# Kernel optimization log

Measured on AMD Instinct MI355X. Metric: run time of the kernel, lower is better.

## Reference

```python
import jax, jax.numpy as jnp
import numpy as np

B, S, Hd = 2, 2048, 2048
NH, DH = 16, 128
FF = 4 * Hd
EPS = 1e-5


def layer_norm(x, g, b):
    mu = jnp.mean(x, axis=-1, keepdims=True)
    var = jnp.mean(jnp.square(x - mu), axis=-1, keepdims=True)
    return (x - mu) * jax.lax.rsqrt(var + EPS) * g + b


def setup_inputs() -> dict:
    key = jax.random.key(0)
    ks = jax.random.split(key, 10)
    s = lambda n: 1.0 / np.sqrt(n)
    return {
        "hidden_states": jax.random.normal(ks[0], (B, S, Hd), jnp.float32),
        "attention_mask": jnp.zeros((B, S), jnp.float32),
        "ln1_g": jnp.ones((Hd,), jnp.float32),
        "ln1_b": jnp.zeros((Hd,), jnp.float32),
        "ln2_g": jnp.ones((Hd,), jnp.float32),
        "ln2_b": jnp.zeros((Hd,), jnp.float32),
        "Wq": jax.random.normal(ks[1], (Hd, NH * DH), jnp.float32) * s(Hd),
        "Wk": jax.random.normal(ks[2], (Hd, NH * DH), jnp.float32) * s(Hd),
        "Wv": jax.random.normal(ks[3], (Hd, NH * DH), jnp.float32) * s(Hd),
        "Wo": jax.random.normal(ks[4], (NH * DH, Hd), jnp.float32) * s(NH * DH),
        "W1": jax.random.normal(ks[5], (Hd, FF), jnp.float32) * s(Hd),
        "b1": jnp.zeros((FF,), jnp.float32),
        "W2": jax.random.normal(ks[6], (FF, Hd), jnp.float32) * s(FF),
        "b2": jnp.zeros((Hd,), jnp.float32),
    }


def reference(hidden_states, attention_mask, ln1_g, ln1_b, ln2_g, ln2_b,
              Wq, Wk, Wv, Wo, W1, b1, W2, b2):
    x = hidden_states
    # --- attention sub-block ---
    h = layer_norm(x, ln1_g, ln1_b)
    q = (h @ Wq).reshape(B, S, NH, DH)
    k = (h @ Wk).reshape(B, S, NH, DH)
    v = (h @ Wv).reshape(B, S, NH, DH)
    scores = jnp.einsum("bqhd,bkhd->bhqk", q, k) / np.sqrt(DH).astype(np.float32)
    scores = scores + attention_mask[:, None, None, :]  # additive mask
    probs = jax.nn.softmax(scores, axis=-1)
    ctx = jnp.einsum("bhqk,bkhd->bqhd", probs, v).reshape(B, S, NH * DH)
    x = x + ctx @ Wo
    # --- MLP sub-block ---
    h = layer_norm(x, ln2_g, ln2_b)
    h = jax.nn.gelu(h @ W1 + b1, approximate=False)
    x = x + h @ W2 + b2
    return x
```

## Files before the change

kernel.cpp:

```cpp
#include <hip/hip_runtime.h>
#include <math.h>

#define B_ 2
#define S_ 2048
#define HD 2048
#define NH_ 16
#define DH_ 128
#define FF_ 8192
#define MROWS (B_*S_)
#define LDQ 6144

typedef __attribute__((ext_vector_type(8))) short bf16x8;
typedef __attribute__((ext_vector_type(4))) short s16x4;
typedef __attribute__((ext_vector_type(4))) float f32x4;

static __device__ __forceinline__ unsigned short f2bf(float f) {
    unsigned u = __float_as_uint(f);
    u += 0x7fffu + ((u >> 16) & 1u);
    return (unsigned short)(u >> 16);
}

static __device__ __forceinline__ unsigned short f2bf_rna(float f) {
    return (unsigned short)((__float_as_uint(f) + 0x8000u) >> 16);
}

static __device__ __forceinline__ void gload_lds16(const void* g, void* lds) {
    __builtin_amdgcn_global_load_lds((const __attribute__((address_space(1))) void*)g,
                                     (__attribute__((address_space(3))) void*)lds, 16, 0, 0);
}

__global__ __launch_bounds__(256) void trcvt_kernel(const float* __restrict__ W,
        short* __restrict__ Wt, int K, int N) {
    __shared__ float tile[64][65];
    int t = threadIdx.x;
    int tr = t >> 4;
    int tc4 = (t & 15) * 4;
    int r0 = blockIdx.y * 64, c0 = blockIdx.x * 64;
    #pragma unroll
    for (int i = 0; i < 4; i++) {
        float4 v = *(const float4*)(W + (size_t)(r0 + tr + 16*i) * N + c0 + tc4);
        tile[tr + 16*i][tc4 + 0] = v.x;
        tile[tr + 16*i][tc4 + 1] = v.y;
        tile[tr + 16*i][tc4 + 2] = v.z;
        tile[tr + 16*i][tc4 + 3] = v.w;
    }
    __syncthreads();
    #pragma unroll
    for (int i = 0; i < 4; i++) {
        int oc = tr + 16*i;
        s16x4 o;
        o.x = (short)f2bf(tile[tc4 + 0][oc]);
        o.y = (short)f2bf(tile[tc4 + 1][oc]);
        o.z = (short)f2bf(tile[tc4 + 2][oc]);
        o.w = (short)f2bf(tile[tc4 + 3][oc]);
        *(s16x4*)(Wt + (size_t)(c0 + oc) * K + r0 + tc4) = o;
    }
}

__global__ __launch_bounds__(256) void vtrans_kernel(const short* __restrict__ qkv,
        short* __restrict__ vT) {
    __shared__ short tile[32][33];
    int t = threadIdx.x;
    int tx = t & 31, ty = t >> 5;
    int c0 = blockIdx.x * 32;
    int r0 = blockIdx.y * 32;
    int b  = blockIdx.z;
    #pragma unroll
    for (int i = 0; i < 4; i++)
        tile[ty + 8*i][tx] = qkv[(size_t)(b*S_ + r0 + ty + 8*i) * LDQ + 4096 + c0 + tx];
    __syncthreads();
    #pragma unroll
    for (int i = 0; i < 4; i++)
        vT[((size_t)(c0 + ty + 8*i) * 2 + b) * S_ + r0 + tx] = tile[tx][ty + 8*i];
}

__global__ __launch_bounds__(256) void ln_kernel(const float* __restrict__ x,
                const float* __restrict__ g, const float* __restrict__ b,
                short* __restrict__ out) {
    int row = blockIdx.x;
    const float* xr = x + (size_t)row * HD;
    short* orow = out + (size_t)row * HD;
    int t = threadIdx.x;

    float4 v0 = ((const float4*)xr)[t];
    float4 v1 = ((const float4*)xr)[t + 256];
    float s  = v0.x + v0.y + v0.z + v0.w + v1.x + v1.y + v1.z + v1.w;
    float ss = v0.x*v0.x + v0.y*v0.y + v0.z*v0.z + v0.w*v0.w
             + v1.x*v1.x + v1.y*v1.y + v1.z*v1.z + v1.w*v1.w;

    #pragma unroll
    for (int off = 1; off < 64; off <<= 1) {
        s  += __shfl_xor(s,  off, 64);
        ss += __shfl_xor(ss, off, 64);
    }
    __shared__ float ws_s[4], ws_q[4];
    int wid = t >> 6;
    if ((t & 63) == 0) { ws_s[wid] = s; ws_q[wid] = ss; }
    __syncthreads();
    s  = ws_s[0] + ws_s[1] + ws_s[2] + ws_s[3];
    ss = ws_q[0] + ws_q[1] + ws_q[2] + ws_q[3];

    float mu  = s * (1.0f / HD);
    float var = ss * (1.0f / HD) - mu * mu;
    float rs  = rsqrtf(var + 1e-5f);

    float4 g0 = ((const float4*)g)[t];
    float4 g1 = ((const float4*)g)[t + 256];
    float4 b0 = ((const float4*)b)[t];
    float4 b1 = ((const float4*)b)[t + 256];
    s16x4 o0, o1;
    o0.x = (short)f2bf((v0.x - mu) * rs * g0.x + b0.x);
    o0.y = (short)f2bf((v0.y - mu) * rs * g0.y + b0.y);
    o0.z = (short)f2bf((v0.z - mu) * rs * g0.z + b0.z);
    o0.w = (short)f2bf((v0.w - mu) * rs * g0.w + b0.w);
    o1.x = (short)f2bf((v1.x - mu) * rs * g1.x + b1.x);
    o1.y = (short)f2bf((v1.y - mu) * rs * g1.y + b1.y);
    o1.z = (short)f2bf((v1.z - mu) * rs * g1.z + b1.z);
    o1.w = (short)f2bf((v1.w - mu) * rs * g1.w + b1.w);
    ((s16x4*)orow)[t]       = o0;
    ((s16x4*)orow)[t + 256] = o1;
}

template<bool PATCH, bool OUTBF16, bool BIAS, bool RES, bool GELU>
__global__ __launch_bounds__(256, 2) void gemm128(
        const short* __restrict__ A, const short* __restrict__ Bt,
        const float* __restrict__ bias, const float* __restrict__ res,
        void* __restrict__ Cout, int M, int N, int K) {
    __shared__ __align__(16) char ldsA[2][128 * 128];
    __shared__ __align__(16) char ldsB[2][128 * 128];

    int tid = threadIdx.x;
    int wave = tid >> 6, lane = tid & 63;
    int l4 = lane >> 4, lm = lane & 15;
    int wm = wave >> 1, wn = wave & 1;

    int bid = blockIdx.x;
    int m0, n0;
    if constexpr (PATCH) {
        int xcd = bid & 7, local = bid >> 3;
        m0 = ((xcd & 3) * 8 + (local & 7)) << 7;
        n0 = ((xcd >> 2) * 8 + (local >> 3)) << 7;
    } else {
        int nx = N >> 7;
        m0 = (bid / nx) << 7; n0 = (bid % nx) << 7;
    }

    const short* Atile = A + (size_t)m0 * K;
    const short* Btile = Bt + (size_t)n0 * K;
    const int NT = K >> 6;

    auto stage = [&](int t, int buf) {
        int tw = (t >= NT) ? t - NT : t;
        const short* gA = Atile + tw * 64;
        const short* gB = Btile + tw * 64;
        #pragma unroll
        for (int s = 0; s < 4; s++) {
            int n = (wave * 4 + s) * 64 + lane;
            int row = n >> 3, c = n & 7;
            int cs = c ^ (row & 7);
            gload_lds16(gA + (size_t)row * K + cs * 8, ldsA[buf] + n * 16);
            gload_lds16(gB + (size_t)row * K + cs * 8, ldsB[buf] + n * 16);
        }
    };

    int ch0 = (l4) ^ (lm & 7);
    int ch1 = (4 | l4) ^ (lm & 7);
    const char* pA = (const char*)ldsA + (wm * 64 + lm) * 128;
    const char* pB = (const char*)ldsB + (wn * 64 + lm) * 128;

    f32x4 acc[4][4] = {};

    stage(0, 0);
    for (int t = 0; t < NT; t++) {
        int buf = t & 1;
        stage(t + 1, buf ^ 1);
        asm volatile("s_waitcnt vmcnt(8)" ::: "memory");
        __builtin_amdgcn_s_barrier();
        __builtin_amdgcn_sched_barrier(0);
        size_t bo = (size_t)buf * 128 * 128;
        __builtin_amdgcn_s_setprio(1);
        #pragma unroll
        for (int kk = 0; kk < 2; kk++) {
            int ch = kk ? ch1 : ch0;
            bf16x8 av[4], bv[4];
            #pragma unroll
            for (int f = 0; f < 4; f++)
                av[f] = *(const bf16x8*)(pA + bo + f * 2048 + ch * 16);
            #pragma unroll
            for (int nn = 0; nn < 4; nn++)
                bv[nn] = *(const bf16x8*)(pB + bo + nn * 2048 + ch * 16);
            #pragma unroll
            for (int f = 0; f < 4; f++)
                #pragma unroll
                for (int nn = 0; nn < 4; nn++)
                    acc[f][nn] = __builtin_amdgcn_mfma_f32_16x16x32_bf16(
                        av[f], bv[nn], acc[f][nn], 0, 0, 0);
        }
        __builtin_amdgcn_s_setprio(0);
        __builtin_amdgcn_s_barrier();
    }
    asm volatile("s_waitcnt vmcnt(0)" ::: "memory");
    __builtin_amdgcn_s_barrier();

    #pragma unroll
    for (int nn = 0; nn < 4; nn++) {
        int colb = n0 + wn * 64 + nn * 16 + lm;
        float bvs = BIAS ? bias[colb] : 0.f;
        #pragma unroll
        for (int m = 0; m < 4; m++) {
            #pragma unroll
            for (int r = 0; r < 4; r++) {
                int row = m0 + wm * 64 + m * 16 + l4 * 4 + r;
                float v = acc[m][nn][r] + bvs;
                if (GELU) {
                    float y = 1.5957691f * (v + 0.044715f * v * v * v);
                    v = v / (1.0f + __expf(-y));
                }
                size_t off = (size_t)row * N + colb;
                if (RES) v += res[off];
                if (OUTBF16) ((short*)Cout)[off] = (short)f2bf(v);
                else         ((float*)Cout)[off] = v;
            }
        }
    }
}

__global__ __launch_bounds__(256) void attn_kernel(
        const short* __restrict__ qkv, const short* __restrict__ vT,
        const float* __restrict__ mask, short* __restrict__ ctx) {
    __shared__ __align__(16) short Ks[64*128];
    __shared__ __align__(16) short Vt[128*64];
    __shared__ __align__(16) short Ps[4][16*72];
    int t = threadIdx.x;
    int wave = t >> 6, lane = t & 63;
    int l4 = lane >> 4, lm = lane & 15;
    int q0 = blockIdx.x * 64, h = blockIdx.y, zb = blockIdx.z;
    const float scale = 0.08838834764831845f;

    bf16x8 aq[4];
    {
        const short* qrow = qkv + (size_t)(zb*S_ + q0 + wave*16 + lm) * LDQ + h*DH_;
        #pragma unroll
        for (int ks = 0; ks < 4; ks++)
            aq[ks] = *(const bf16x8*)(qrow + ks*32 + l4*8);
    }

    float m_r[4], l_r[4];
    #pragma unroll
    for (int r = 0; r < 4; r++) { m_r[r] = -INFINITY; l_r[r] = 0.f; }
    f32x4 o[8];
    #pragma unroll
    for (int i = 0; i < 8; i++) o[i] = (f32x4){0.f, 0.f, 0.f, 0.f};

    for (int kv0 = 0; kv0 < S_; kv0 += 64) {
        __syncthreads();
        #pragma unroll
        for (int L = 0; L < 4; L++) {
            int c = (wave*4 + L)*64 + lane;
            int krow = c >> 4, kc = c & 15;
            int ksrc = (kc & 8) | ((kc ^ (krow & 7)) & 7);
            gload_lds16(qkv + (size_t)(zb*S_ + kv0 + krow)*LDQ + 2048 + h*DH_ + ksrc*8,
                        (char*)Ks + c*16);
            int drow = c >> 3, dc = c & 7;
            int dsrc = dc ^ (drow & 7);
            gload_lds16(vT + ((size_t)(h*DH_ + drow)*2 + zb)*S_ + kv0 + dsrc*8,
                        (char*)Vt + c*16);
        }
        __syncthreads();

        f32x4 s[4];
        #pragma unroll
        for (int nb = 0; nb < 4; nb++) s[nb] = (f32x4){0.f, 0.f, 0.f, 0.f};
        __builtin_amdgcn_s_setprio(1);
        #pragma unroll
        for (int nb = 0; nb < 4; nb++) {
            int row = nb*16 + lm;
            #pragma unroll
            for (int ks = 0; ks < 4; ks++) {
                bf16x8 bk = *(const bf16x8*)((const char*)Ks +
                              ((row*256 + ks*64 + l4*16) ^ ((row & 7) << 4)));
                s[nb] = __builtin_amdgcn_mfma_f32_16x16x32_bf16(aq[ks], bk, s[nb], 0, 0, 0);
            }
        }
        __builtin_amdgcn_s_setprio(0);

        float mk[4];
        #pragma unroll
        for (int nb = 0; nb < 4; nb++) mk[nb] = mask[(size_t)zb*S_ + kv0 + nb*16 + lm];

        float pv_[4][4], pm[4];
        float need = -1e30f;
        #pragma unroll
        for (int r = 0; r < 4; r++) {
            float vmax = -INFINITY;
            #pragma unroll
            for (int nb = 0; nb < 4; nb++) {
                float v = fmaf(s[nb][r], scale, mk[nb]);
                pv_[r][nb] = v;
                vmax = fmaxf(vmax, v);
            }
            vmax = fmaxf(vmax, __shfl_xor(vmax, 1, 64));
            vmax = fmaxf(vmax, __shfl_xor(vmax, 2, 64));
            vmax = fmaxf(vmax, __shfl_xor(vmax, 4, 64));
            vmax = fmaxf(vmax, __shfl_xor(vmax, 8, 64));
            pm[r] = vmax;
            need = fmaxf(need, vmax - m_r[r]);
        }
        if (!__all(need <= 8.0f)) {
            float fac[4];
            #pragma unroll
            for (int r = 0; r < 4; r++) {
                float nm = fmaxf(m_r[r], pm[r]);
                fac[r] = __expf(m_r[r] - nm);
                l_r[r] *= fac[r];
                m_r[r] = nm;
            }
            #pragma unroll
            for (int i = 0; i < 8; i++)
                #pragma unroll
                for (int r = 0; r < 4; r++) o[i][r] *= fac[r];
        }
        #pragma unroll
        for (int r = 0; r < 4; r++) {
            float ps = 0.f;
            #pragma unroll
            for (int nb = 0; nb < 4; nb++) {
                float e = __expf(pv_[r][nb] - m_r[r]);
                pv_[r][nb] = e;
                ps += e;
            }
            ps += __shfl_xor(ps, 1, 64);
            ps += __shfl_xor(ps, 2, 64);
            ps += __shfl_xor(ps, 4, 64);
            ps += __shfl_xor(ps, 8, 64);
            l_r[r] += ps;
        }

        short* Pw = (short*)Ps[wave];
        #pragma unroll
        for (int r = 0; r < 4; r++)
            #pragma unroll
            for (int nb = 0; nb < 4; nb++)
                Pw[(l4*4 + r)*72 + nb*16 + lm] = (short)f2bf_rna(pv_[r][nb]);

        __builtin_amdgcn_s_setprio(1);
        #pragma unroll
        for (int ks = 0; ks < 2; ks++) {
            bf16x8 ap = *(const bf16x8*)(Pw + lm*72 + ks*32 + l4*8);
            #pragma unroll
            for (int nd = 0; nd < 8; nd++) {
                int d = nd*16 + lm;
                bf16x8 bvv = *(const bf16x8*)((const char*)Vt +
                              (((d*128) + ks*64 + l4*16) ^ ((d & 7) << 4)));
                o[nd] = __builtin_amdgcn_mfma_f32_16x16x32_bf16(ap, bvv, o[nd], 0, 0, 0);
            }
        }
        __builtin_amdgcn_s_setprio(0);
    }

    float inv[4];
    #pragma unroll
    for (int r = 0; r < 4; r++) inv[r] = 1.0f / l_r[r];
    #pragma unroll
    for (int nd = 0; nd < 8; nd++) {
        #pragma unroll
        for (int r = 0; r < 4; r++) {
            size_t row = (size_t)(zb*S_ + q0 + wave*16 + l4*4 + r);
            ctx[row * HD + h*DH_ + nd*16 + lm] = (short)f2bf(o[nd][r] * inv[r]);
        }
    }
}

extern "C" void kernel_launch(void* const* d_in, const int* in_sizes, int n_in,
                              void* d_out, int out_size, void* d_ws, size_t ws_size,
                              hipStream_t stream) {
    const float* x      = (const float*)d_in[0];
    const float* mask   = (const float*)d_in[1];
    const float* ln1_g  = (const float*)d_in[2];
    const float* ln1_b  = (const float*)d_in[3];
    const float* ln2_g  = (const float*)d_in[4];
    const float* ln2_b  = (const float*)d_in[5];
    const float* Wq     = (const float*)d_in[6];
    const float* Wk     = (const float*)d_in[7];
    const float* Wv     = (const float*)d_in[8];
    const float* Wo     = (const float*)d_in[9];
    const float* W1     = (const float*)d_in[10];
    const float* b1     = (const float*)d_in[11];
    const float* W2     = (const float*)d_in[12];
    const float* b2     = (const float*)d_in[13];
    float* out = (float*)d_out;

    char* ws = (char*)d_ws;
    size_t off = 0;
    const size_t WSQ  = (size_t)HD * HD * 2;
    const size_t WFF  = (size_t)HD * FF_ * 2;
    const size_t ACTB = (size_t)MROWS * HD * 2;
    short* WqkvT = (short*)(ws + off); off += 3 * WSQ;
    short* WoT   = (short*)(ws + off); off += WSQ;
    short* W1T   = (short*)(ws + off); off += WFF;
    short* W2T   = (short*)(ws + off); off += WFF;
    short* hb    = (short*)(ws + off); off += ACTB;
    short* qkv   = (short*)(ws + off); off += (size_t)MROWS * LDQ * 2;
    short* vTb   = (short*)(ws + off); off += (size_t)HD * B_ * S_ * 2;
    float* x1    = (float*)(ws + off); off += (size_t)MROWS * HD * 4;
    short* cb    = WqkvT;
    short* act   = qkv;

    dim3 blk(256);

    trcvt_kernel<<<dim3(HD/64,  HD/64),  blk, 0, stream>>>(Wq, WqkvT,                 HD, HD);
    trcvt_kernel<<<dim3(HD/64,  HD/64),  blk, 0, stream>>>(Wk, WqkvT + (size_t)HD*HD, HD, HD);
    trcvt_kernel<<<dim3(HD/64,  HD/64),  blk, 0, stream>>>(Wv, WqkvT + (size_t)2*HD*HD, HD, HD);
    trcvt_kernel<<<dim3(HD/64,  HD/64),  blk, 0, stream>>>(Wo, WoT, HD, HD);
    trcvt_kernel<<<dim3(FF_/64, HD/64),  blk, 0, stream>>>(W1, W1T, HD, FF_);
    trcvt_kernel<<<dim3(HD/64,  FF_/64), blk, 0, stream>>>(W2, W2T, FF_, HD);

    ln_kernel<<<MROWS, blk, 0, stream>>>(x, ln1_g, ln1_b, hb);

    gemm128<false,true,false,false,false><<<dim3((MROWS/128)*(LDQ/128)), 256, 0, stream>>>(
        hb, WqkvT, nullptr, nullptr, qkv, MROWS, LDQ, HD);

    vtrans_kernel<<<dim3(HD/32, S_/32, B_), blk, 0, stream>>>(qkv, vTb);

    attn_kernel<<<dim3(S_/64, NH_, B_), blk, 0, stream>>>(qkv, vTb, mask, cb);

    gemm128<true,false,false,true,false><<<dim3((MROWS/128)*(HD/128)), 256, 0, stream>>>(
        cb, WoT, nullptr, x, x1, MROWS, HD, HD);

    ln_kernel<<<MROWS, blk, 0, stream>>>(x1, ln2_g, ln2_b, hb);

    gemm128<false,true,true,false,true><<<dim3((MROWS/128)*(FF_/128)), 256, 0, stream>>>(
        hb, W1T, b1, nullptr, act, MROWS, FF_, HD);

    gemm128<true,false,true,true,false><<<dim3((MROWS/128)*(HD/128)), 256, 0, stream>>>(
        act, W2T, b2, x1, out, MROWS, HD, FF_);
}
```

Before: 768.2 us.

## Double-buffer K/V tiles in attention to overlap global loads with MFMA

The attention kernel now keeps two LDS buffers for K and V and issues the async global-to-LDS loads for the next tile before computing on the current one. It waits only on the older batch of loads (vmcnt(8)) and uses explicit barriers, so load latency can hide behind the QK and PV MFMAs. The last iteration stages a redundant wrapped-around tile to keep the wait count uniform, which adds one extra tile of traffic. LDS use doubles to about 72KB, which may lower occupancy.

```diff
diff --git a/kernel.cpp b/kernel.cpp
--- a/kernel.cpp
+++ b/kernel.cpp
@@ -228,14 +228,15 @@
 __global__ __launch_bounds__(256) void attn_kernel(
         const short* __restrict__ qkv, const short* __restrict__ vT,
         const float* __restrict__ mask, short* __restrict__ ctx) {
-    __shared__ __align__(16) short Ks[64*128];
-    __shared__ __align__(16) short Vt[128*64];
+    __shared__ __align__(16) short Ks[2][64*128];
+    __shared__ __align__(16) short Vt[2][128*64];
     __shared__ __align__(16) short Ps[4][16*72];
     int t = threadIdx.x;
     int wave = t >> 6, lane = t & 63;
     int l4 = lane >> 4, lm = lane & 15;
     int q0 = blockIdx.x * 64, h = blockIdx.y, zb = blockIdx.z;
     const float scale = 0.08838834764831845f;
+    const int NT = S_ / 64;
 
     bf16x8 aq[4];
     {
@@ -245,28 +246,40 @@
             aq[ks] = *(const bf16x8*)(qrow + ks*32 + l4*8);
     }
 
-    float m_r[4], l_r[4];
-    #pragma unroll
-    for (int r = 0; r < 4; r++) { m_r[r] = -INFINITY; l_r[r] = 0.f; }
-    f32x4 o[8];
-    #pragma unroll
-    for (int i = 0; i < 8; i++) o[i] = (f32x4){0.f, 0.f, 0.f, 0.f};
-
-    for (int kv0 = 0; kv0 < S_; kv0 += 64) {
-        __syncthreads();
+    auto stageKV = [&](int ti, int buf) {
+        int tw = (ti >= NT) ? ti - NT : ti;
+        int kv0 = tw * 64;
         #pragma unroll
         for (int L = 0; L < 4; L++) {
             int c = (wave*4 + L)*64 + lane;
             int krow = c >> 4, kc = c & 15;
             int ksrc = (kc & 8) | ((kc ^ (krow & 7)) & 7);
             gload_lds16(qkv + (size_t)(zb*S_ + kv0 + krow)*LDQ + 2048 + h*DH_ + ksrc*8,
-                        (char*)Ks + c*16);
+                        (char*)Ks[buf] + c*16);
             int drow = c >> 3, dc = c & 7;
             int dsrc = dc ^ (drow & 7);
             gload_lds16(vT + ((size_t)(h*DH_ + drow)*2 + zb)*S_ + kv0 + dsrc*8,
-                        (char*)Vt + c*16);
-        }
-        __syncthreads();
+                        (char*)Vt[buf] + c*16);
+        }
+    };
+
+    float m_r[4], l_r[4];
+    #pragma unroll
+    for (int r = 0; r < 4; r++) { m_r[r] = -INFINITY; l_r[r] = 0.f; }
+    f32x4 o[8];
+    #pragma unroll
+    for (int i = 0; i < 8; i++) o[i] = (f32x4){0.f, 0.f, 0.f, 0.f};
+
+    stageKV(0, 0);
+    for (int ti = 0; ti < NT; ti++) {
+        int buf = ti & 1;
+        int kv0 = ti * 64;
+        stageKV(ti + 1, buf ^ 1);
+        asm volatile("s_waitcnt vmcnt(8)" ::: "memory");
+        __builtin_amdgcn_s_barrier();
+        __builtin_amdgcn_sched_barrier(0);
+        const char* Kb = (const char*)Ks[buf];
+        const char* Vb = (const char*)Vt[buf];
 
         f32x4 s[4];
         #pragma unroll
@@ -277,7 +290,7 @@
             int row = nb*16 + lm;
             #pragma unroll
             for (int ks = 0; ks < 4; ks++) {
-                bf16x8 bk = *(const bf16x8*)((const char*)Ks +
+                bf16x8 bk = *(const bf16x8*)(Kb +
                               ((row*256 + ks*64 + l4*16) ^ ((row & 7) << 4)));
                 s[nb] = __builtin_amdgcn_mfma_f32_16x16x32_bf16(aq[ks], bk, s[nb], 0, 0, 0);
             }
@@ -350,13 +363,16 @@
             #pragma unroll
             for (int nd = 0; nd < 8; nd++) {
                 int d = nd*16 + lm;
-                bf16x8 bvv = *(const bf16x8*)((const char*)Vt +
+                bf16x8 bvv = *(const bf16x8*)(Vb +
                               (((d*128) + ks*64 + l4*16) ^ ((d & 7) << 4)));
                 o[nd] = __builtin_amdgcn_mfma_f32_16x16x32_bf16(ap, bvv, o[nd], 0, 0, 0);
             }
         }
         __builtin_amdgcn_s_setprio(0);
-    }
+        __builtin_amdgcn_s_barrier();
+    }
+    asm volatile("s_waitcnt vmcnt(0)" ::: "memory");
+    __builtin_amdgcn_s_barrier();
 
     float inv[4];
     #pragma unroll
```

After: 765.4 us. About the same (-0.4%).
